# Kernel tuning notes

Measured on AMD Instinct MI355X. Metric: run time of the kernel, lower is better.

Reference implementation:

```python
import jax, jax.numpy as jnp
import numpy as np

N_USERS = 100_000
N_ITEMS = 200_000
N = N_USERS + N_ITEMS
D = 64
N_INTER = 5_000_000
N_LAYERS = 3
BATCH = 4096


def setup_inputs() -> dict:
    rng = np.random.default_rng(0)
    uu = rng.integers(0, N_USERS, N_INTER)            # user node ids
    ii = rng.integers(0, N_ITEMS, N_INTER) + N_USERS  # item node ids (offset)
    # degrees over the bipartite graph, then D^{-1/2} A D^{-1/2} edge values
    deg = np.bincount(uu, minlength=N).astype(np.float32) + \
          np.bincount(ii, minlength=N).astype(np.float32)
    deg[deg == 0] = 1.0
    vals = (1.0 / np.sqrt(deg[uu] * deg[ii])).astype(np.float32)
    rows = np.concatenate([uu, ii]).astype(np.int32)   # symmetric COO
    cols = np.concatenate([ii, uu]).astype(np.int32)
    vals2 = np.concatenate([vals, vals]).astype(np.float32)

    key = jax.random.key(0)
    k1, k2, k3, k4 = jax.random.split(key, 4)
    return {
        "u": jax.random.randint(k1, (BATCH,), 0, N_USERS),
        "i": jax.random.randint(k2, (BATCH,), 0, N_ITEMS),
        "adj_rows": jnp.asarray(rows),
        "adj_cols": jnp.asarray(cols),
        "adj_vals": jnp.asarray(vals2),
        "U_emb": 0.01 * jax.random.normal(k3, (N_USERS, D), dtype=jnp.float32),
        "V_emb": 0.01 * jax.random.normal(k4, (N_ITEMS, D), dtype=jnp.float32),
    }


def _spmm(rows, cols, vals, E):
    # sparse (N,N) @ dense (N,D) via gather-scale-scatter
    return jax.ops.segment_sum(vals[:, None] * E[cols], rows, num_segments=N)


def reference(u, i, adj_rows, adj_cols, adj_vals, U_emb, V_emb):
    E = jnp.concatenate([U_emb, V_emb], axis=0)  # (N, D) = E0
    acc = E
    cur = E
    for _ in range(N_LAYERS):
        cur = _spmm(adj_rows, adj_cols, adj_vals, cur)
        acc = acc + cur
    Ef = acc / jnp.asarray(N_LAYERS + 1, E.dtype)  # mean of E0..EK
    return jnp.sum(Ef[u] * Ef[N_USERS + i], axis=1)  # (B,) scores
```

## Files before the change

### kernel.cpp

```cpp
#include <hip/hip_runtime.h>

#define DIMS 64
#define SCAN_CHUNK 2048
#define BSHIFT 10
#define BROWS (1 << BSHIFT)
#define NB_MAX 304
#define BCAP 65536
#define SCAP 24
#define SPITCH 25
#define PA_THREADS 256
#define PA_K 4
#define PA_HALFROUND (PA_THREADS / 2 * PA_K)
#define PA_HCHUNK 4096
#define PB_THREADS 512
#define SENTINEL 0xFFFFFFFFu

__device__ __forceinline__ int ld_nt_int(const int* p) {
  return __builtin_nontemporal_load(p);
}

__device__ __forceinline__ float bf_lo(unsigned u) {
  return __uint_as_float(u << 16);
}
__device__ __forceinline__ float bf_hi(unsigned u) {
  return __uint_as_float(u & 0xFFFF0000u);
}
__device__ __forceinline__ unsigned f2bf(float f) {
  unsigned u = __float_as_uint(f);
  return (u + 0x7FFFu + ((u >> 16) & 1u)) >> 16;
}

__global__ __launch_bounds__(256) void init_es_kernel(
    const float* __restrict__ U, const float* __restrict__ V,
    const float* __restrict__ rs, unsigned short* __restrict__ Es,
    int nU_elems, int total_elems) {
  int i4 = (blockIdx.x * blockDim.x + threadIdx.x) * 4;
  if (i4 >= total_elems) return;
  float4 v = (i4 < nU_elems)
      ? *reinterpret_cast<const float4*>(U + i4)
      : *reinterpret_cast<const float4*>(V + (i4 - nU_elems));
  float s = rs[i4 >> 6];
  uint2 o;
  o.x = f2bf(v.x * s) | (f2bf(v.y * s) << 16);
  o.y = f2bf(v.z * s) | (f2bf(v.w * s) << 16);
  *reinterpret_cast<uint2*>(Es + i4) = o;
}

__global__ __launch_bounds__(PA_THREADS) void pass_a_kernel(
    const int* __restrict__ rows, const int* __restrict__ cols,
    unsigned* __restrict__ temp, int* __restrict__ gcur, int nnz, int nb) {
  __shared__ unsigned stage[NB_MAX * SPITCH];
  __shared__ int scnt[NB_MAX];
  for (int b = threadIdx.x; b < nb; b += PA_THREADS) scnt[b] = 0;
  __syncthreads();

  const int half = nnz >> 1;
  const int u0 = blockIdx.x * PA_HCHUNK;
  const int u1 = min(half, u0 + PA_HCHUNK);
  const int i0 = half + blockIdx.x * PA_HCHUNK;
  const int i1 = min(nnz, i0 + PA_HCHUNK);
  const int tid = threadIdx.x;

  for (int rd = 0; rd < PA_HCHUNK / PA_HALFROUND; ++rd) {
    int base, lim;
    if (tid < PA_THREADS / 2) {
      base = u0 + rd * PA_HALFROUND + tid * PA_K;
      lim = u1;
    } else {
      base = i0 + rd * PA_HALFROUND + (tid - PA_THREADS / 2) * PA_K;
      lim = i1;
    }

    unsigned packed[PA_K];
    int bkt[PA_K];
    unsigned pend = 0;
    if (base + PA_K <= lim && ((base & 3) == 0)) {
      int4 r4 = *reinterpret_cast<const int4*>(rows + base);
      int4 c4 = *reinterpret_cast<const int4*>(cols + base);
      int rr[PA_K] = {r4.x, r4.y, r4.z, r4.w};
      int cc[PA_K] = {c4.x, c4.y, c4.z, c4.w};
#pragma unroll
      for (int k = 0; k < PA_K; ++k) {
        bkt[k] = rr[k] >> BSHIFT;
        packed[k] = ((unsigned)(rr[k] & (BROWS - 1)) << 19) | (unsigned)cc[k];
      }
      pend = (1u << PA_K) - 1;
    } else {
#pragma unroll
      for (int k = 0; k < PA_K; ++k) {
        int e = base + k;
        if (e < lim) {
          int r = rows[e];
          int c = cols[e];
          bkt[k] = r >> BSHIFT;
          packed[k] = ((unsigned)(r & (BROWS - 1)) << 19) | (unsigned)c;
          pend |= 1u << k;
        }
      }
    }

    for (;;) {
#pragma unroll
      for (int k = 0; k < PA_K; ++k) {
        if (pend & (1u << k)) {
          int idx = atomicAdd(&scnt[bkt[k]], 1);
          if (idx < SCAP) {
            stage[bkt[k] * SPITCH + idx] = packed[k];
            pend &= ~(1u << k);
          } else {
            atomicAdd(&scnt[bkt[k]], -1);
          }
        }
      }
      __syncthreads();
      for (int bb = threadIdx.x; bb < nb; bb += PA_THREADS) {
        int cval = scnt[bb];
        if (cval >= 16) {
          int pos = atomicAdd(&gcur[bb], 16);
          unsigned v[16];
#pragma unroll
          for (int k = 0; k < 16; ++k) v[k] = stage[bb * SPITCH + k];
          uint4* dst = reinterpret_cast<uint4*>(&temp[pos]);
          dst[0] = make_uint4(v[0], v[1], v[2], v[3]);
          dst[1] = make_uint4(v[4], v[5], v[6], v[7]);
          dst[2] = make_uint4(v[8], v[9], v[10], v[11]);
          dst[3] = make_uint4(v[12], v[13], v[14], v[15]);
          for (int k = 0; k < cval - 16; ++k)
            stage[bb * SPITCH + k] = stage[bb * SPITCH + 16 + k];
          scnt[bb] = cval - 16;
        }
      }
      int pend_total = __syncthreads_count(pend ? 1 : 0);
      if (pend_total == 0) break;
    }
  }
  __syncthreads();
  for (int bb = threadIdx.x; bb < nb; bb += PA_THREADS) {
    int cval = scnt[bb];
    if (cval > 0) {
      int pos = atomicAdd(&gcur[bb], 16);
      for (int k = 0; k < 16; ++k)
        temp[pos + k] = (k < cval) ? stage[bb * SPITCH + k] : SENTINEL;
    }
  }
}

__global__ __launch_bounds__(512) void hist_bucket_kernel(
    const unsigned* __restrict__ temp, const int* __restrict__ gcur,
    int* __restrict__ cnt, int n) {
  __shared__ int lcnt[BROWS];
  int b = blockIdx.x;
  int base_row = b << BSHIFT;
  int nrows = min(BROWS, n - base_row);
  for (int r = threadIdx.x; r < BROWS; r += 512) lcnt[r] = 0;
  __syncthreads();
  int start = b * BCAP, end = gcur[b];
  for (int i = start + threadIdx.x; i < end; i += 512) {
    unsigned ent = temp[i];
    if (ent != SENTINEL) atomicAdd(&lcnt[ent >> 19], 1);
  }
  __syncthreads();
  for (int r = threadIdx.x; r < nrows; r += 512)
    cnt[base_row + r] = lcnt[r];
}

__global__ __launch_bounds__(256) void scan_phase1(
    const int* __restrict__ cnt, int* __restrict__ block_sums, int n) {
  __shared__ int sdata[256];
  int base = blockIdx.x * SCAN_CHUNK;
  int sum = 0;
#pragma unroll
  for (int k = 0; k < 8; ++k) {
    int idx = base + k * 256 + threadIdx.x;
    if (idx < n) sum += cnt[idx];
  }
  sdata[threadIdx.x] = sum;
  __syncthreads();
  for (int s = 128; s > 0; s >>= 1) {
    if (threadIdx.x < s) sdata[threadIdx.x] += sdata[threadIdx.x + s];
    __syncthreads();
  }
  if (threadIdx.x == 0) block_sums[blockIdx.x] = sdata[0];
}

__global__ __launch_bounds__(256) void scan_phase2(
    int* __restrict__ block_sums, int n_blocks, int* __restrict__ row_ptr, int n) {
  __shared__ int tmp[256];
  int v = (threadIdx.x < n_blocks) ? block_sums[threadIdx.x] : 0;
  tmp[threadIdx.x] = v;
  __syncthreads();
  for (int offs = 1; offs < 256; offs <<= 1) {
    int t = (threadIdx.x >= offs) ? tmp[threadIdx.x - offs] : 0;
    __syncthreads();
    tmp[threadIdx.x] += t;
    __syncthreads();
  }
  if (threadIdx.x < n_blocks) block_sums[threadIdx.x] = tmp[threadIdx.x] - v;
  if (threadIdx.x == 0) row_ptr[n] = tmp[255];
}

__global__ __launch_bounds__(256) void scan_phase3(
    const int* __restrict__ cnt, const int* __restrict__ block_sums,
    int* __restrict__ row_ptr, int n) {
  __shared__ int tmp[256];
  __shared__ int s_carry;
  int base = blockIdx.x * SCAN_CHUNK;
  if (threadIdx.x == 0) s_carry = block_sums[blockIdx.x];
  __syncthreads();
#pragma unroll 1
  for (int k = 0; k < 8; ++k) {
    int idx = base + k * 256 + threadIdx.x;
    int v = (idx < n) ? cnt[idx] : 0;
    tmp[threadIdx.x] = v;
    __syncthreads();
    for (int offs = 1; offs < 256; offs <<= 1) {
      int t = (threadIdx.x >= offs) ? tmp[threadIdx.x - offs] : 0;
      __syncthreads();
      tmp[threadIdx.x] += t;
      __syncthreads();
    }
    int incl = tmp[threadIdx.x];
    int carry = s_carry;
    if (idx < n) row_ptr[idx] = carry + incl - v;
    __syncthreads();
    if (threadIdx.x == 0) s_carry = carry + tmp[255];
    __syncthreads();
  }
}

__global__ __launch_bounds__(256) void rs_kernel(
    const int* __restrict__ cnt, float* __restrict__ rs,
    float* __restrict__ rs2, float* __restrict__ irs, int n) {
  int i = blockIdx.x * blockDim.x + threadIdx.x;
  if (i < n) {
    float d = (float)cnt[i];
    float r = (d > 0.0f) ? 1.0f / sqrtf(d) : 1.0f;
    rs[i] = r;
    rs2[i] = r * r;
    irs[i] = (d > 0.0f) ? sqrtf(d) : 1.0f;
  }
}

__global__ __launch_bounds__(256) void bucket_init_kernel(
    int* __restrict__ gcur, int nb) {
  int b = blockIdx.x * blockDim.x + threadIdx.x;
  if (b < nb) gcur[b] = b * BCAP;
}

__global__ __launch_bounds__(PB_THREADS) void pass_b_kernel(
    const unsigned* __restrict__ temp, const int* __restrict__ gcur,
    const int* __restrict__ row_ptr, int* __restrict__ csr_col, int nb, int n) {
  __shared__ int ldscur[BROWS];
  for (int b = blockIdx.x; b < nb; b += gridDim.x) {
    int base_row = b << BSHIFT;
    int nrows = min(BROWS, n - base_row);
    for (int r = threadIdx.x; r < nrows; r += PB_THREADS)
      ldscur[r] = row_ptr[base_row + r];
    __syncthreads();
    int start = b * BCAP, end = gcur[b];
    for (int i = start + threadIdx.x; i < end; i += PB_THREADS) {
      unsigned ent = temp[i];
      if (ent != SENTINEL) {
        int col = (int)(ent & 0x7FFFFu);
        int rlow = (int)(ent >> 19);
        int p = atomicAdd(&ldscur[rlow], 1);
        csr_col[p] = col;
      }
    }
    __syncthreads();
  }
}

__global__ __launch_bounds__(256) void spmm_kernel(
    const int* __restrict__ row_ptr, const int* __restrict__ csr_col,
    const float* __restrict__ rs2, const uint2* __restrict__ cur2,
    uint2* __restrict__ next2, int n_rows) {
  int row  = blockIdx.x * (blockDim.x >> 6) + (threadIdx.x >> 6);
  int lane = threadIdx.x & 63;
  int q    = lane >> 4;
  int sub  = lane & 15;
  if (row >= n_rows) return;
  int start = row_ptr[row];
  int end   = row_ptr[row + 1];
  float4 acc = make_float4(0.0f, 0.0f, 0.0f, 0.0f);
  for (int e = start; e < end; e += 16) {
    int c[4];
    bool m[4];
    uint2 g[4];
#pragma unroll
    for (int k = 0; k < 4; ++k) {
      int idx = e + 4 * k + q;
      m[k] = idx < end;
      c[k] = ld_nt_int(csr_col + (m[k] ? idx : (end - 1)));
    }
#pragma unroll
    for (int k = 0; k < 4; ++k) g[k] = cur2[c[k] * 16 + sub];
#pragma unroll
    for (int k = 0; k < 4; ++k) {
      unsigned gx = m[k] ? g[k].x : 0u;
      unsigned gy = m[k] ? g[k].y : 0u;
      acc.x += bf_lo(gx); acc.y += bf_hi(gx);
      acc.z += bf_lo(gy); acc.w += bf_hi(gy);
    }
  }
#pragma unroll
  for (int offs = 16; offs <= 32; offs <<= 1) {
    acc.x += __shfl_xor(acc.x, offs, 64);
    acc.y += __shfl_xor(acc.y, offs, 64);
    acc.z += __shfl_xor(acc.z, offs, 64);
    acc.w += __shfl_xor(acc.w, offs, 64);
  }
  if (q == 0) {
    float s = rs2[row];
    uint2 o;
    o.x = f2bf(acc.x * s) | (f2bf(acc.y * s) << 16);
    o.y = f2bf(acc.z * s) | (f2bf(acc.w * s) << 16);
    next2[row * 16 + sub] = o;
  }
}

__global__ __launch_bounds__(256) void batch_spmm_kernel(
    const int* __restrict__ u, const int* __restrict__ it,
    const int* __restrict__ row_ptr, const int* __restrict__ csr_col,
    const float* __restrict__ rs, const uint2* __restrict__ cur2,
    float* __restrict__ accU, float* __restrict__ accI, int batch, int nU) {
  int t    = blockIdx.x * (blockDim.x >> 6) + (threadIdx.x >> 6);
  int lane = threadIdx.x & 63;
  int q    = lane >> 4;
  int sub  = lane & 15;
  if (t >= 2 * batch) return;
  int b = t >> 1;
  bool uside = (t & 1) == 0;
  int row = uside ? u[b] : (it[b] + nU);
  int start = row_ptr[row];
  int end   = row_ptr[row + 1];
  float4 acc = make_float4(0.0f, 0.0f, 0.0f, 0.0f);
  for (int e = start; e < end; e += 16) {
    int c[4];
    bool m[4];
    uint2 g[4];
#pragma unroll
    for (int k = 0; k < 4; ++k) {
      int idx = e + 4 * k + q;
      m[k] = idx < end;
      c[k] = ld_nt_int(csr_col + (m[k] ? idx : (end - 1)));
    }
#pragma unroll
    for (int k = 0; k < 4; ++k) g[k] = cur2[c[k] * 16 + sub];
#pragma unroll
    for (int k = 0; k < 4; ++k) {
      unsigned gx = m[k] ? g[k].x : 0u;
      unsigned gy = m[k] ? g[k].y : 0u;
      acc.x += bf_lo(gx); acc.y += bf_hi(gx);
      acc.z += bf_lo(gy); acc.w += bf_hi(gy);
    }
  }
#pragma unroll
  for (int offs = 16; offs <= 32; offs <<= 1) {
    acc.x += __shfl_xor(acc.x, offs, 64);
    acc.y += __shfl_xor(acc.y, offs, 64);
    acc.z += __shfl_xor(acc.z, offs, 64);
    acc.w += __shfl_xor(acc.w, offs, 64);
  }
  if (q == 0) {
    float s = rs[row];
    float* dst = (uside ? accU : accI) + (size_t)b * DIMS + sub * 4;
    float4 old = *reinterpret_cast<float4*>(dst);
    old.x += acc.x * s; old.y += acc.y * s;
    old.z += acc.z * s; old.w += acc.w * s;
    *reinterpret_cast<float4*>(dst) = old;
  }
}

__global__ __launch_bounds__(256) void gather0_kernel(
    const int* __restrict__ u, const int* __restrict__ it,
    const float* __restrict__ U, const float* __restrict__ V,
    float* __restrict__ accU, float* __restrict__ accI, int batch) {
  int b    = blockIdx.x * (blockDim.x >> 6) + (threadIdx.x >> 6);
  int lane = threadIdx.x & 63;
  if (b >= batch) return;
  accU[b * DIMS + lane] = U[u[b] * DIMS + lane];
  accI[b * DIMS + lane] = V[it[b] * DIMS + lane];
}

__global__ __launch_bounds__(256) void gather_s_kernel(
    const int* __restrict__ u, const int* __restrict__ it,
    const unsigned short* __restrict__ curS, const float* __restrict__ irs,
    float* __restrict__ accU, float* __restrict__ accI, int batch, int nU) {
  int b    = blockIdx.x * (blockDim.x >> 6) + (threadIdx.x >> 6);
  int lane = threadIdx.x & 63;
  if (b >= batch) return;
  int ru = u[b];
  int ri = it[b] + nU;
  accU[b * DIMS + lane] +=
      __uint_as_float((unsigned)curS[ru * DIMS + lane] << 16) * irs[ru];
  accI[b * DIMS + lane] +=
      __uint_as_float((unsigned)curS[ri * DIMS + lane] << 16) * irs[ri];
}

__global__ __launch_bounds__(256) void score_kernel(
    const float* __restrict__ accU, const float* __restrict__ accI,
    float* __restrict__ out, int batch) {
  int b    = blockIdx.x * (blockDim.x >> 6) + (threadIdx.x >> 6);
  int lane = threadIdx.x & 63;
  if (b >= batch) return;
  float v = accU[b * DIMS + lane] * accI[b * DIMS + lane];
  for (int offs = 32; offs > 0; offs >>= 1) v += __shfl_down(v, offs, 64);
  if (lane == 0) out[b] = v * (1.0f / 16.0f);
}

extern "C" void kernel_launch(void* const* d_in, const int* in_sizes, int n_in,
                              void* d_out, int out_size, void* d_ws, size_t ws_size,
                              hipStream_t stream) {
  const int*   u     = (const int*)d_in[0];
  const int*   it    = (const int*)d_in[1];
  const int*   arows = (const int*)d_in[2];
  const int*   acols = (const int*)d_in[3];
  const float* U     = (const float*)d_in[5];
  const float* V     = (const float*)d_in[6];

  const int batch = in_sizes[0];
  const int nnz   = in_sizes[2];
  const int nU    = in_sizes[5] / DIMS;
  const int nV    = in_sizes[6] / DIMS;
  const int N     = nU + nV;
  const int n_scan_blocks = (N + SCAN_CHUNK - 1) / SCAN_CHUNK;
  const int NB    = (N + BROWS - 1) >> BSHIFT;
  const size_t esbytes = (size_t)N * DIMS * 2;
  const size_t tbytes  = (size_t)NB * BCAP * 4;
  const size_t xbytes  = tbytes > esbytes ? tbytes : esbytes;

  const int big_half = nnz - nnz / 2;
  const int PA_B = (big_half + PA_HCHUNK - 1) / PA_HCHUNK;

  char*  ws  = (char*)d_ws;
  size_t off = 0;
  auto take = [&](size_t bytes) -> void* {
    void* p = ws + off;
    off = (off + bytes + 255) & ~(size_t)255;
    return p;
  };
  int*     cnt        = (int*)take((size_t)N * 4);
  float*   rs         = (float*)take((size_t)N * 4);
  float*   rs2        = (float*)take((size_t)N * 4);
  float*   irs        = (float*)take((size_t)N * 4);
  int*     row_ptr    = (int*)take((size_t)(N + 1) * 4);
  int*     block_sums = (int*)take((size_t)256 * 4);
  int*     gcur       = (int*)take((size_t)NB * 4);
  int*     csr_col    = (int*)take((size_t)nnz * 4);
  char*    X          = (char*)take(xbytes);
  unsigned short* bufB = (unsigned short*)take(esbytes);
  float*   accU       = (float*)take((size_t)batch * DIMS * 4);
  float*   accI       = (float*)take((size_t)batch * DIMS * 4);
  unsigned* temp      = (unsigned*)X;
  unsigned short* bufA = (unsigned short*)X;

  bucket_init_kernel<<<(NB + 255) / 256, 256, 0, stream>>>(gcur, NB);
  pass_a_kernel<<<PA_B, PA_THREADS, 0, stream>>>(arows, acols, temp, gcur, nnz, NB);
  hist_bucket_kernel<<<NB, 512, 0, stream>>>(temp, gcur, cnt, N);
  scan_phase1<<<n_scan_blocks, 256, 0, stream>>>(cnt, block_sums, N);
  scan_phase2<<<1, 256, 0, stream>>>(block_sums, n_scan_blocks, row_ptr, N);
  scan_phase3<<<n_scan_blocks, 256, 0, stream>>>(cnt, block_sums, row_ptr, N);
  rs_kernel<<<(N + 255) / 256, 256, 0, stream>>>(cnt, rs, rs2, irs, N);
  pass_b_kernel<<<NB, PB_THREADS, 0, stream>>>(temp, gcur, row_ptr,
                                               csr_col, NB, N);

  gather0_kernel<<<(batch + 3) / 4, 256, 0, stream>>>(u, it, U, V, accU, accI,
                                                      batch);

  {
    int total = N * DIMS;
    int t4 = total / 4;
    init_es_kernel<<<(t4 + 255) / 256, 256, 0, stream>>>(U, V, rs, bufA,
                                                         nU * DIMS, total);
  }

  unsigned short* cur = bufA;
  unsigned short* nxt = bufB;
  for (int layer = 0; layer < 2; ++layer) {
    spmm_kernel<<<(N + 3) / 4, 256, 0, stream>>>(
        row_ptr, csr_col, rs2, (const uint2*)cur, (uint2*)nxt, N);
    gather_s_kernel<<<(batch + 3) / 4, 256, 0, stream>>>(u, it, nxt, irs, accU,
                                                         accI, batch, nU);
    unsigned short* t = cur; cur = nxt; nxt = t;
  }
  batch_spmm_kernel<<<(2 * batch + 3) / 4, 256, 0, stream>>>(
      u, it, row_ptr, csr_col, rs, (const uint2*)cur, accU, accI, batch, nU);

  score_kernel<<<(batch + 3) / 4, 256, 0, stream>>>(accU, accI, (float*)d_out, batch);
}
```

Before: 923.0 us.

## Read only first half of symmetric COO and emit both directions in bucketing

```diff
diff --git a/kernel.cpp b/kernel.cpp
--- a/kernel.cpp
+++ b/kernel.cpp
@@ -6,12 +6,12 @@
 #define BROWS (1 << BSHIFT)
 #define NB_MAX 304
 #define BCAP 65536
-#define SCAP 24
-#define SPITCH 25
+#define SCAP 40
+#define SPITCH 41
 #define PA_THREADS 256
 #define PA_K 4
-#define PA_HALFROUND (PA_THREADS / 2 * PA_K)
-#define PA_HCHUNK 4096
+#define PA_ROUND (PA_THREADS * PA_K)
+#define PA_CHUNK 4096
 #define PB_THREADS 512
 #define SENTINEL 0xFFFFFFFFu
 
@@ -55,53 +55,49 @@
   __syncthreads();
 
   const int half = nnz >> 1;
-  const int u0 = blockIdx.x * PA_HCHUNK;
-  const int u1 = min(half, u0 + PA_HCHUNK);
-  const int i0 = half + blockIdx.x * PA_HCHUNK;
-  const int i1 = min(nnz, i0 + PA_HCHUNK);
-  const int tid = threadIdx.x;
-
-  for (int rd = 0; rd < PA_HCHUNK / PA_HALFROUND; ++rd) {
-    int base, lim;
-    if (tid < PA_THREADS / 2) {
-      base = u0 + rd * PA_HALFROUND + tid * PA_K;
-      lim = u1;
-    } else {
-      base = i0 + rd * PA_HALFROUND + (tid - PA_THREADS / 2) * PA_K;
-      lim = i1;
-    }
-
-    unsigned packed[PA_K];
-    int bkt[PA_K];
+  const int c0 = blockIdx.x * PA_CHUNK;
+  const int c1 = min(half, c0 + PA_CHUNK);
+
+  for (int rd = 0; rd < PA_CHUNK / PA_ROUND; ++rd) {
+    int base = c0 + rd * PA_ROUND + threadIdx.x * PA_K;
+
+    unsigned packed[2 * PA_K];
+    int bkt[2 * PA_K];
     unsigned pend = 0;
-    if (base + PA_K <= lim && ((base & 3) == 0)) {
+    if (base + PA_K <= c1) {
       int4 r4 = *reinterpret_cast<const int4*>(rows + base);
       int4 c4 = *reinterpret_cast<const int4*>(cols + base);
       int rr[PA_K] = {r4.x, r4.y, r4.z, r4.w};
       int cc[PA_K] = {c4.x, c4.y, c4.z, c4.w};
 #pragma unroll
       for (int k = 0; k < PA_K; ++k) {
-        bkt[k] = rr[k] >> BSHIFT;
-        packed[k] = ((unsigned)(rr[k] & (BROWS - 1)) << 19) | (unsigned)cc[k];
+        bkt[2 * k] = rr[k] >> BSHIFT;
+        packed[2 * k] =
+            ((unsigned)(rr[k] & (BROWS - 1)) << 19) | (unsigned)cc[k];
+        bkt[2 * k + 1] = cc[k] >> BSHIFT;
+        packed[2 * k + 1] =
+            ((unsigned)(cc[k] & (BROWS - 1)) << 19) | (unsigned)rr[k];
       }
-      pend = (1u << PA_K) - 1;
+      pend = (1u << (2 * PA_K)) - 1;
     } else {
 #pragma unroll
       for (int k = 0; k < PA_K; ++k) {
         int e = base + k;
-        if (e < lim) {
+        if (e < c1) {
           int r = rows[e];
           int c = cols[e];
-          bkt[k] = r >> BSHIFT;
-          packed[k] = ((unsigned)(r & (BROWS - 1)) << 19) | (unsigned)c;
-          pend |= 1u << k;
+          bkt[2 * k] = r >> BSHIFT;
+          packed[2 * k] = ((unsigned)(r & (BROWS - 1)) << 19) | (unsigned)c;
+          bkt[2 * k + 1] = c >> BSHIFT;
+          packed[2 * k + 1] = ((unsigned)(c & (BROWS - 1)) << 19) | (unsigned)r;
+          pend |= 3u << (2 * k);
         }
       }
     }
 
     for (;;) {
 #pragma unroll
-      for (int k = 0; k < PA_K; ++k) {
+      for (int k = 0; k < 2 * PA_K; ++k) {
         if (pend & (1u << k)) {
           int idx = atomicAdd(&scnt[bkt[k]], 1);
           if (idx < SCAP) {
@@ -116,18 +112,21 @@
       for (int bb = threadIdx.x; bb < nb; bb += PA_THREADS) {
         int cval = scnt[bb];
         if (cval >= 16) {
-          int pos = atomicAdd(&gcur[bb], 16);
-          unsigned v[16];
-#pragma unroll
-          for (int k = 0; k < 16; ++k) v[k] = stage[bb * SPITCH + k];
-          uint4* dst = reinterpret_cast<uint4*>(&temp[pos]);
-          dst[0] = make_uint4(v[0], v[1], v[2], v[3]);
-          dst[1] = make_uint4(v[4], v[5], v[6], v[7]);
-          dst[2] = make_uint4(v[8], v[9], v[10], v[11]);
-          dst[3] = make_uint4(v[12], v[13], v[14], v[15]);
-          for (int k = 0; k < cval - 16; ++k)
-            stage[bb * SPITCH + k] = stage[bb * SPITCH + 16 + k];
-          scnt[bb] = cval - 16;
+          while (cval >= 16) {
+            int pos = atomicAdd(&gcur[bb], 16);
+            unsigned v[16];
+#pragma unroll
+            for (int k = 0; k < 16; ++k) v[k] = stage[bb * SPITCH + k];
+            uint4* dst = reinterpret_cast<uint4*>(&temp[pos]);
+            dst[0] = make_uint4(v[0], v[1], v[2], v[3]);
+            dst[1] = make_uint4(v[4], v[5], v[6], v[7]);
+            dst[2] = make_uint4(v[8], v[9], v[10], v[11]);
+            dst[3] = make_uint4(v[12], v[13], v[14], v[15]);
+            for (int k = 0; k < cval - 16; ++k)
+              stage[bb * SPITCH + k] = stage[bb * SPITCH + 16 + k];
+            cval -= 16;
+          }
+          scnt[bb] = cval;
         }
       }
       int pend_total = __syncthreads_count(pend ? 1 : 0);
@@ -430,8 +429,8 @@
   const size_t tbytes  = (size_t)NB * BCAP * 4;
   const size_t xbytes  = tbytes > esbytes ? tbytes : esbytes;
 
-  const int big_half = nnz - nnz / 2;
-  const int PA_B = (big_half + PA_HCHUNK - 1) / PA_HCHUNK;
+  const int half  = nnz >> 1;
+  const int PA_B  = (half + PA_CHUNK - 1) / PA_CHUNK;
 
   char*  ws  = (char*)d_ws;
   size_t off = 0;
```

Result: faster. 857.5 us (-7.1%).
